# Kernel tuning notes

Measured on AMD Instinct MI355X. Metric: run time of the kernel, lower is better.

## Reference

```python
import jax, jax.numpy as jnp
import numpy as np

D_MODEL = 2048
N_HEAD = 16
HEAD_DIM = D_MODEL // N_HEAD
D_FF = 8192
SEQ = 2048
PAST = 2048
BATCH = 2
LN_EPS = 1e-5


def setup_inputs() -> dict:
    key = jax.random.key(0)
    ks = jax.random.split(key, 16)
    s = 0.02  # weight init scale
    return {
        "x": jax.random.normal(ks[0], (SEQ, BATCH, D_MODEL), jnp.float32),
        "k_cache": jax.random.normal(ks[1], (PAST, BATCH, N_HEAD, HEAD_DIM), jnp.float32),
        "v_cache": jax.random.normal(ks[2], (PAST, BATCH, N_HEAD, HEAD_DIM), jnp.float32),
        "mask": jnp.zeros((SEQ, PAST + SEQ), jnp.float32),
        "q_w": jax.random.normal(ks[3], (D_MODEL, D_MODEL), jnp.float32) * s,
        "q_b": jnp.zeros((D_MODEL,), jnp.float32),
        "k_w": jax.random.normal(ks[4], (D_MODEL, D_MODEL), jnp.float32) * s,
        "k_b": jnp.zeros((D_MODEL,), jnp.float32),
        "v_w": jax.random.normal(ks[5], (D_MODEL, D_MODEL), jnp.float32) * s,
        "v_b": jnp.zeros((D_MODEL,), jnp.float32),
        "o_w": jax.random.normal(ks[6], (D_MODEL, D_MODEL), jnp.float32) * s,
        "o_b": jnp.zeros((D_MODEL,), jnp.float32),
        "ln1_g": jnp.ones((D_MODEL,), jnp.float32),
        "ln1_b": jnp.zeros((D_MODEL,), jnp.float32),
        "ln2_g": jnp.ones((D_MODEL,), jnp.float32),
        "ln2_b": jnp.zeros((D_MODEL,), jnp.float32),
        "w1": jax.random.normal(ks[7], (D_MODEL, D_FF), jnp.float32) * s,
        "b1": jnp.zeros((D_FF,), jnp.float32),
        "w2": jax.random.normal(ks[8], (D_FF, D_MODEL), jnp.float32) * s,
        "b2": jnp.zeros((D_MODEL,), jnp.float32),
    }


def _layernorm(y, g, b):
    m = jnp.mean(y, axis=-1, keepdims=True)
    v = jnp.var(y, axis=-1, keepdims=True)  # biased var, matches torch LayerNorm
    return (y - m) * jax.lax.rsqrt(v + LN_EPS) * g + b


def reference(x, k_cache, v_cache, mask, q_w, q_b, k_w, k_b, v_w, v_b, o_w, o_b,
              ln1_g, ln1_b, ln2_g, ln2_b, w1, b1, w2, b2):
    S, B, D = x.shape
    H, hd = N_HEAD, HEAD_DIM

    x_norm = _layernorm(x, ln1_g, ln1_b)
    q = (x_norm @ q_w + q_b).reshape(S, B, H, hd)
    k = (x_norm @ k_w + k_b).reshape(S, B, H, hd)
    v = (x_norm @ v_w + v_b).reshape(S, B, H, hd)

    k_full = jnp.concatenate([k_cache, k], axis=0)  # [T,B,H,hd], T = past+S
    v_full = jnp.concatenate([v_cache, v], axis=0)

    # scores: [B,H,S,T]
    scores = jnp.einsum('sbhd,tbhd->bhst', q, k_full) / (hd ** 0.5)
    scores = scores + mask  # mask [S,T] broadcasts over B,H
    attn = jax.nn.softmax(scores, axis=-1)
    out = jnp.einsum('bhst,tbhd->sbhd', attn, v_full).reshape(S, B, D)
    x = x + out @ o_w + o_b

    h = _layernorm(x, ln2_g, ln2_b)
    x = x + jax.nn.gelu(h @ w1 + b1, approximate=False) @ w2 + b2
    return (x, k_full, v_full)
```

## Files before the change

### kernel.cpp

```cpp
#include <hip/hip_runtime.h>
#include <hip/hip_bf16.h>


typedef __bf16 bf16x8 __attribute__((ext_vector_type(8)));
typedef float f32x4 __attribute__((ext_vector_type(4)));
typedef float f32x16 __attribute__((ext_vector_type(16)));
typedef unsigned int u32;

__device__ __forceinline__ unsigned short f2bf(float f) {
  union { float f; unsigned u; } v; v.f = f;
  return (unsigned short)((v.u + 0x7FFFu + ((v.u >> 16) & 1u)) >> 16);
}

__device__ __forceinline__ void gl16(const void* g, void* l) {
  __builtin_amdgcn_global_load_lds((__attribute__((address_space(1))) void*)g,
                                   (__attribute__((address_space(3))) void*)l,
                                   16, 0, 0);
}

__global__ __launch_bounds__(256) void ln_k(const float* __restrict__ X,
                                            const float* __restrict__ G,
                                            const float* __restrict__ Bb,
                                            unsigned short* __restrict__ Y) {
  const int row = blockIdx.x;
  const int tid = threadIdx.x;
  const float4* xr = (const float4*)(X + (size_t)row * 2048);
  const float4 xa = xr[tid], xb = xr[tid + 256];
  float s = xa.x + xa.y + xa.z + xa.w + xb.x + xb.y + xb.z + xb.w;
  float q = xa.x * xa.x + xa.y * xa.y + xa.z * xa.z + xa.w * xa.w +
            xb.x * xb.x + xb.y * xb.y + xb.z * xb.z + xb.w * xb.w;
  for (int off = 32; off; off >>= 1) {
    s += __shfl_xor(s, off);
    q += __shfl_xor(q, off);
  }
  __shared__ float red[8];
  const int wv = tid >> 6, ln = tid & 63;
  if (ln == 0) { red[wv] = s; red[4 + wv] = q; }
  __syncthreads();
  s = red[0] + red[1] + red[2] + red[3];
  q = red[4] + red[5] + red[6] + red[7];
  const float mean = s * (1.f / 2048.f);
  const float rstd = rsqrtf(q * (1.f / 2048.f) - mean * mean + 1e-5f);
  const float4 g0 = ((const float4*)G)[tid], g1 = ((const float4*)G)[tid + 256];
  const float4 b0 = ((const float4*)Bb)[tid], b1 = ((const float4*)Bb)[tid + 256];
  ushort4 o0, o1;
  o0.x = f2bf((xa.x - mean) * rstd * g0.x + b0.x);
  o0.y = f2bf((xa.y - mean) * rstd * g0.y + b0.y);
  o0.z = f2bf((xa.z - mean) * rstd * g0.z + b0.z);
  o0.w = f2bf((xa.w - mean) * rstd * g0.w + b0.w);
  o1.x = f2bf((xb.x - mean) * rstd * g1.x + b1.x);
  o1.y = f2bf((xb.y - mean) * rstd * g1.y + b1.y);
  o1.z = f2bf((xb.z - mean) * rstd * g1.z + b1.z);
  o1.w = f2bf((xb.w - mean) * rstd * g1.w + b1.w);
  ((ushort4*)(Y + (size_t)row * 2048))[tid] = o0;
  ((ushort4*)(Y + (size_t)row * 2048))[tid + 256] = o1;
}

__global__ __launch_bounds__(256) void wconvT(const float* __restrict__ W,
                                              unsigned short* __restrict__ Wt,
                                              int K, int N) {
  __shared__ float tl[32][33];
  const int k0 = blockIdx.x * 32, n0 = blockIdx.y * 32;
  const int x = threadIdx.x & 31, y = threadIdx.x >> 5;
  for (int i = 0; i < 4; ++i)
    tl[y + i * 8][x] = W[(size_t)(k0 + y + i * 8) * N + n0 + x];
  __syncthreads();
  for (int i = 0; i < 4; ++i)
    Wt[(size_t)(n0 + y + i * 8) * K + k0 + x] = f2bf(tl[x][y + i * 8]);
}

__global__ __launch_bounds__(256) void kpack(const float* __restrict__ src,
                                             unsigned short* __restrict__ dstb,
                                             float* __restrict__ dstf) {
  const size_t e = ((size_t)blockIdx.x * 256 + threadIdx.x) * 4;
  const int r = (int)(e >> 11), c = (int)(e & 2047);
  const int t = r >> 1, b = r & 1, h = c >> 7, d = c & 127;
  const float4 v = *(const float4*)(src + e);
  ushort4 o;
  o.x = f2bf(v.x); o.y = f2bf(v.y); o.z = f2bf(v.z); o.w = f2bf(v.w);
  *(ushort4*)(dstb + ((size_t)((b * 16 + h) * 4096 + t)) * 128 + d) = o;
  *(float4*)(dstf + (size_t)r * 2048 + c) = v;
}

__global__ __launch_bounds__(256) void vtrans(const float* __restrict__ src,
                                              unsigned short* __restrict__ dstb,
                                              float* __restrict__ dstf) {
  __shared__ float tl[32][33];
  const int bh = blockIdx.z;
  const int b = bh >> 4, h = bh & 15;
  const int t0 = blockIdx.x * 32, d0 = blockIdx.y * 32;
  const int x = threadIdx.x & 31, y = threadIdx.x >> 5;
  for (int i = 0; i < 4; ++i) {
    const int t = t0 + y + i * 8, d = d0 + x;
    const float v = src[((size_t)(t * 2 + b) * 16 + h) * 128 + d];
    tl[y + i * 8][x] = v;
    dstf[((size_t)(t * 2 + b) * 16 + h) * 128 + d] = v;
  }
  __syncthreads();
  for (int i = 0; i < 4; ++i) {
    const int d = d0 + y + i * 8, t = t0 + x;
    dstb[((size_t)bh * 128 + d) * 4096 + t] = f2bf(tl[x][y + i * 8]);
  }
}

__global__ __launch_bounds__(256) void mask0_k(const float* __restrict__ mask,
                                               u32* __restrict__ flags) {
  const float4* p = (const float4*)mask + (size_t)blockIdx.x * 8192 + threadIdx.x;
  int nz = 0;
#pragma unroll
  for (int i = 0; i < 32; ++i) {
    const float4 v = p[i * 256];
    nz |= (v.x != 0.f) | (v.y != 0.f) | (v.z != 0.f) | (v.w != 0.f);
  }
  const int r = __syncthreads_or(nz);
  if (threadIdx.x == 0) flags[blockIdx.x] = (u32)r;
}

template <int TAG, int EPI>
__global__ __launch_bounds__(256) void gemm_bt(
    const unsigned short* __restrict__ A, const unsigned short* __restrict__ Bt,
    const float* __restrict__ bias, const float* __restrict__ Rsd,
    float* __restrict__ Cf, int N, int K) {
  __shared__ unsigned short sA[128 * 64];
  __shared__ unsigned short sB[128 * 64];
  const int tid = threadIdx.x;
  const int wv = tid >> 6, ln = tid & 63;
  const int nwg = gridDim.x;
  const int bid = blockIdx.x;
  const int wk = (bid & 7) * (nwg >> 3) + (bid >> 3);
  const int m0 = (wk & 31) * 128, n0 = (wk >> 5) * 128;
  const int wm = (wv >> 1) * 64, wn = (wv & 1) * 64;
  f32x4 acc[4][4] = {};
  const int nk = K >> 6;
  for (int kt = 0; kt < nk; ++kt) {
    __syncthreads();
#pragma unroll
    for (int c = 0; c < 4; ++c) {
      const int base = (wv * 4 + c) * 1024;
      const int o = base + ln * 16;
      const int row = o >> 7;
      const int xx = o ^ ((row & 7) << 4);
      gl16((const char*)A + ((size_t)(m0 + row) * K + (size_t)kt * 64) * 2 + (xx & 127),
           (char*)sA + base);
      gl16((const char*)Bt + ((size_t)(n0 + row) * K + (size_t)kt * 64) * 2 + (xx & 127),
           (char*)sB + base);
    }
    __syncthreads();
#pragma unroll
    for (int kk = 0; kk < 2; ++kk) {
      bf16x8 af[4], bf[4];
#pragma unroll
      for (int i = 0; i < 4; ++i) {
        const int ra = wm + i * 16 + (ln & 15);
        int aa = (ra << 7) + ((ln >> 4) << 4) + kk * 64;
        aa ^= (ra & 7) << 4;
        af[i] = *(const bf16x8*)((const char*)sA + aa);
        const int rb = wn + i * 16 + (ln & 15);
        int bb = (rb << 7) + ((ln >> 4) << 4) + kk * 64;
        bb ^= (rb & 7) << 4;
        bf[i] = *(const bf16x8*)((const char*)sB + bb);
      }
#pragma unroll
      for (int i = 0; i < 4; ++i)
#pragma unroll
        for (int j = 0; j < 4; ++j)
          acc[i][j] = __builtin_amdgcn_mfma_f32_16x16x32_bf16(af[i], bf[j],
                                                              acc[i][j], 0, 0, 0);
    }
  }
  const int lr = (ln >> 4) << 2, lc = ln & 15;
#pragma unroll
  for (int i = 0; i < 4; ++i) {
#pragma unroll
    for (int j = 0; j < 4; ++j) {
      const int n = n0 + wn + j * 16 + lc;
      const float bv = bias[n];
#pragma unroll
      for (int r = 0; r < 4; ++r) {
        const int m = m0 + wm + i * 16 + lr + r;
        float v = acc[i][j][r] + bv + Rsd[(size_t)m * N + n];
        Cf[(size_t)m * N + n] = v;
      }
    }
  }
}

template <int TAG, int EPI>
__global__ __launch_bounds__(512) void gemm8p(
    const unsigned short* __restrict__ A, const unsigned short* __restrict__ Bt,
    const float* __restrict__ bias, const float* __restrict__ bias2,
    const float* __restrict__ bias3,
    float* __restrict__ Cf, unsigned short* __restrict__ Cb,
    float* __restrict__ of2, unsigned short* __restrict__ pb2,
    unsigned short* __restrict__ pb3, int N, int K) {
  __shared__ unsigned short sA[2][256 * 64];
  __shared__ unsigned short sB[2][256 * 64];
  const int tid = threadIdx.x;
  const int wv = tid >> 6, ln = tid & 63;
  const int wm = wv >> 2, wn = wv & 3;
  const int nwg = gridDim.x;
  const int bid = blockIdx.x;
  const int wk = (bid & 7) * (nwg >> 3) + (bid >> 3);
  const int m0 = (wk & 15) * 256, n0 = (wk >> 4) * 256;
  const int NT = K >> 6, NI = NT >> 1;

  f32x4 acc[8][4] = {};
  bf16x8 af[4][2], bfr[2][2];

  auto ST = [&](int t, int which, int bb) {
    if (t >= NT) return;
    const unsigned short* G = (which < 2) ? A : Bt;
    const int base0 = ((which < 2) ? m0 : n0) + (which & 1) * 128;
    char* dst = (char*)((which < 2) ? &sA[bb][0] : &sB[bb][0]) + (which & 1) * 16384;
    const size_t kb = (size_t)t * 64;
#pragma unroll
    for (int c = 0; c < 2; ++c) {
      const int o = tid * 16 + c * 8192;
      const int row = o >> 7;
      const int cb = (o & 127) ^ ((row & 7) << 4);
      gl16((const char*)G + ((size_t)(base0 + row) * K + kb) * 2 + cb, dst + o);
    }
  };
  auto LDA = [&](int bb, int mh) {
    const char* base = (const char*)&sA[bb][0];
#pragma unroll
    for (int i = 0; i < 4; ++i) {
      const int r = wm * 128 + mh * 64 + i * 16 + (ln & 15);
#pragma unroll
      for (int kk = 0; kk < 2; ++kk) {
        int aa = (r << 7) + ((ln >> 4) << 4) + kk * 64;
        aa ^= (r & 7) << 4;
        af[i][kk] = *(const bf16x8*)(base + aa);
      }
    }
  };
  auto LDB = [&](int bb, int nh) {
    const char* base = (const char*)&sB[bb][0];
#pragma unroll
    for (int j = 0; j < 2; ++j) {
      const int r = wn * 64 + nh * 32 + j * 16 + (ln & 15);
#pragma unroll
      for (int kk = 0; kk < 2; ++kk) {
        int aa = (r << 7) + ((ln >> 4) << 4) + kk * 64;
        aa ^= (r & 7) << 4;
        bfr[j][kk] = *(const bf16x8*)(base + aa);
      }
    }
  };
  auto MM = [&](int mh, int nh) {
    __builtin_amdgcn_s_setprio(1);
#pragma unroll
    for (int i = 0; i < 4; ++i)
#pragma unroll
      for (int j = 0; j < 2; ++j)
#pragma unroll
        for (int kk = 0; kk < 2; ++kk)
          acc[mh * 4 + i][nh * 2 + j] = __builtin_amdgcn_mfma_f32_16x16x32_bf16(
              af[i][kk], bfr[j][kk], acc[mh * 4 + i][nh * 2 + j], 0, 0, 0);
    __builtin_amdgcn_s_setprio(0);
  };
#define BAR() __builtin_amdgcn_s_barrier()
#define VM2() asm volatile("s_waitcnt vmcnt(2)" ::: "memory")
#define VM0() asm volatile("s_waitcnt vmcnt(0)" ::: "memory")

  ST(0, 0, 0); ST(0, 1, 0); ST(0, 2, 0); ST(0, 3, 0); ST(1, 0, 1);
  VM2();
  BAR();

#pragma unroll 1
  for (int it = 0; it < NI; ++it) {
    const int t1 = 2 * it + 1, t2 = 2 * it + 2, t3 = 2 * it + 3;
    const bool lastit = (it == NI - 1);
    LDA(0, 0); LDB(0, 0); ST(t1, 1, 1); BAR(); MM(0, 0); BAR();
    LDB(0, 1);            ST(t1, 2, 1); BAR(); MM(0, 1); BAR();
    LDA(0, 1);            ST(t1, 3, 1); BAR(); MM(1, 1); BAR();
    LDB(0, 0);            ST(t2, 0, 0); BAR(); MM(1, 0);
    if (lastit) VM0(); else VM2();
    BAR();
    LDA(1, 0); LDB(1, 0); ST(t2, 1, 0); BAR(); MM(0, 0); BAR();
    LDB(1, 1);            ST(t2, 2, 0); BAR(); MM(0, 1); BAR();
    LDA(1, 1);            ST(t2, 3, 0); BAR(); MM(1, 1); BAR();
    LDB(1, 0);            ST(t3, 0, 1); BAR(); MM(1, 0);
    if (!lastit) VM2();
    BAR();
  }
#undef BAR
#undef VM2
#undef VM0

  const int lr = (ln >> 4) << 2, lc = ln & 15;
  if (EPI == 0) {
    const int seg = n0 >> 11;
    const float* bp = seg == 0 ? bias : (seg == 1 ? bias2 : bias3);
#pragma unroll
    for (int f = 0; f < 8; ++f) {
#pragma unroll
      for (int j = 0; j < 4; ++j) {
        const int nn = (n0 & 2047) + wn * 64 + j * 16 + lc;
        const int h = nn >> 7, d = nn & 127;
        const float bv = bp[nn];
#pragma unroll
        for (int r = 0; r < 4; ++r) {
          const int m = m0 + wm * 128 + f * 16 + lr + r;
          const int s = m >> 1, b = m & 1;
          const float v = acc[f][j][r] + bv;
          if (seg == 0) {
            Cb[((size_t)(b * 16 + h) * 2048 + s) * 128 + d] = f2bf(v);
          } else if (seg == 1) {
            pb2[((size_t)(b * 16 + h) * 4096 + 2048 + s) * 128 + d] = f2bf(v);
            Cf[((size_t)((2048 + s) * 2 + b) * 16 + h) * 128 + d] = v;
          } else {
            pb3[((size_t)(b * 16 + h) * 128 + d) * 4096 + 2048 + s] = f2bf(v);
            of2[((size_t)((2048 + s) * 2 + b) * 16 + h) * 128 + d] = v;
          }
        }
      }
    }
  } else {
#pragma unroll
    for (int f = 0; f < 8; ++f) {
#pragma unroll
      for (int j = 0; j < 4; ++j) {
        const int n = n0 + wn * 64 + j * 16 + lc;
        const float bv = bias[n];
#pragma unroll
        for (int r = 0; r < 4; ++r) {
          const int m = m0 + wm * 128 + f * 16 + lr + r;
          float v = acc[f][j][r] + bv;
          v = 0.5f * v * (1.f + erff(v * 0.7071067811865476f));
          Cb[(size_t)m * N + n] = f2bf(v);
        }
      }
    }
  }
}

__global__ __launch_bounds__(256, 2) void attn2(
    const unsigned short* __restrict__ Q,
    const unsigned short* __restrict__ Kf,
    const unsigned short* __restrict__ Vt,
    const float* __restrict__ mask,
    const u32* __restrict__ flags,
    unsigned short* __restrict__ ctx) {
  __shared__ unsigned short sK[2][64 * 128];
  __shared__ unsigned short sV[2][128 * 64];
  const int tid = threadIdx.x;
  const int wv = tid >> 6;
  const int ln = tid & 63;
  const int q = ln & 31;
  const int hi = ln >> 5;
  const int sw = (q & 7) << 4;
  const int bh = blockIdx.y;
  const int s0w = blockIdx.x * 128 + wv * 32;

  const int mnz = __syncthreads_or((int)flags[tid]);

  bf16x8 qreg[8];
  {
    const char* qsrc = (const char*)Q +
        ((size_t)bh * 2048 + s0w + q) * 256 + (hi << 4);
#pragma unroll
    for (int kk = 0; kk < 8; ++kk) qreg[kk] = *(const bf16x8*)(qsrc + kk * 32);
  }

  const char* Kc = (const char*)Kf + (size_t)bh * 4096 * 256;
  const char* Vc = (const char*)Vt + (size_t)bh * 128 * 8192;

  auto STAGE = [&](int t0, int bi) {
#pragma unroll
    for (int is = 0; is < 4; ++is) {
      const int oo = tid * 16 + is * 4096;
      const int kr = oo >> 8, kc = oo & 255;
      gl16(Kc + (size_t)(t0 + kr) * 256 + (kc ^ ((kr & 7) << 4)),
           (char*)sK[bi] + oo);
      const int vr = oo >> 7, vc = oo & 127;
      gl16(Vc + (size_t)vr * 8192 + (size_t)t0 * 2 + (vc ^ ((vr & 7) << 4)),
           (char*)sV[bi] + oo);
    }
  };

  f32x16 acc[4] = {};
  float m = -1e30f, l = 0.f;
  const float KLOG = 0.127517445f;

  STAGE(0, 0);
  for (int it = 0; it < 64; ++it) {
    const int cur = it & 1;
    __syncthreads();
    if (it < 63) STAGE((it + 1) * 64, cur ^ 1);

    const char* kb = (const char*)sK[cur];
    const char* vb = (const char*)sV[cur];

    f32x16 sc[2];
#pragma unroll
    for (int st = 0; st < 2; ++st) {
      f32x16 z = {};
      __builtin_amdgcn_s_setprio(1);
#pragma unroll
      for (int kk = 0; kk < 8; ++kk) {
        const bf16x8 kf8 = *(const bf16x8*)(
            kb + (((st * 32 + q) << 8) + (((kk << 5) + (hi << 4)) ^ sw)));
        z = __builtin_amdgcn_mfma_f32_32x32x16_bf16(kf8, qreg[kk], z, 0, 0, 0);
      }
      __builtin_amdgcn_s_setprio(0);
      sc[st] = z;
    }

    if (mnz) {
      const float rs = 11.313708498984761f;
#pragma unroll
      for (int st = 0; st < 2; ++st)
#pragma unroll
        for (int r = 0; r < 16; ++r) {
          const int t = it * 64 + st * 32 + ((r & 3) + ((r >> 2) << 3) + (hi << 2));
          sc[st][r] = fmaf(mask[(size_t)(s0w + q) * 4096 + t], rs, sc[st][r]);
        }
    }

    float pmax = sc[0][0];
#pragma unroll
    for (int st = 0; st < 2; ++st)
#pragma unroll
      for (int r = 0; r < 16; ++r) pmax = fmaxf(pmax, sc[st][r]);
    pmax = fmaxf(pmax, __shfl_xor(pmax, 32));
    if (__any(pmax > m + 90.5f)) {
      const float mn = fmaxf(m, pmax);
      const float corr = exp2f((m - mn) * KLOG);
      m = mn; l *= corr;
#pragma unroll
      for (int d4 = 0; d4 < 4; ++d4)
#pragma unroll
        for (int e = 0; e < 16; ++e) acc[d4][e] *= corr;
    }
    const float mk = m * KLOG;
    float rsum = 0.f;
#pragma unroll
    for (int st = 0; st < 2; ++st)
#pragma unroll
      for (int r = 0; r < 16; ++r) {
        const float e = exp2f(fmaf(sc[st][r], KLOG, -mk));
        sc[st][r] = e;
        rsum += e;
      }
    rsum += __shfl_xor(rsum, 32);
    l += rsum;

    bf16x8 pw[4];
#pragma unroll
    for (int kk = 0; kk < 4; ++kk) {
      const int st = kk >> 1, rb = (kk & 1) * 8;
      u32 w0, w1, w2, w3;
      asm("v_cvt_pk_bf16_f32 %0, %1, %2" : "=v"(w0) : "v"(sc[st][rb + 0]), "v"(sc[st][rb + 1]));
      asm("v_cvt_pk_bf16_f32 %0, %1, %2" : "=v"(w1) : "v"(sc[st][rb + 2]), "v"(sc[st][rb + 3]));
      asm("v_cvt_pk_bf16_f32 %0, %1, %2" : "=v"(w2) : "v"(sc[st][rb + 4]), "v"(sc[st][rb + 5]));
      asm("v_cvt_pk_bf16_f32 %0, %1, %2" : "=v"(w3) : "v"(sc[st][rb + 6]), "v"(sc[st][rb + 7]));
      asm("v_permlane32_swap_b32 %0, %1" : "+v"(w0), "+v"(w2));
      asm("v_permlane32_swap_b32 %0, %1" : "+v"(w1), "+v"(w3));
      union { u32 u[4]; bf16x8 b; } pk;
      pk.u[0] = w0; pk.u[1] = w1; pk.u[2] = w2; pk.u[3] = w3;
      pw[kk] = pk.b;
    }

#pragma unroll
    for (int d4 = 0; d4 < 4; ++d4) {
      __builtin_amdgcn_s_setprio(1);
#pragma unroll
      for (int kk = 0; kk < 4; ++kk) {
        const bf16x8 vf8 = *(const bf16x8*)(
            vb + (((d4 * 32 + q) << 7) + (((kk << 5) + (hi << 4)) ^ sw)));
        acc[d4] = __builtin_amdgcn_mfma_f32_32x32x16_bf16(vf8, pw[kk], acc[d4], 0, 0, 0);
      }
      __builtin_amdgcn_s_setprio(0);
    }
  }

  const float inv = 1.f / l;
  const int b = bh >> 4, h = bh & 15;
  unsigned short* crow = ctx + ((size_t)(s0w + q) * 2 + b) * 2048 + h * 128;
#pragma unroll
  for (int d4 = 0; d4 < 4; ++d4)
#pragma unroll
    for (int r = 0; r < 16; ++r) {
      const int d = d4 * 32 + (r & 3) + ((r >> 2) << 3) + (hi << 2);
      crow[d] = f2bf(acc[d4][r] * inv);
    }
}

extern "C" void kernel_launch(void* const* d_in, const int* in_sizes, int n_in,
                              void* d_out, int out_size, void* d_ws, size_t ws_size,
                              hipStream_t stream) {
  const float* x    = (const float*)d_in[0];
  const float* kc   = (const float*)d_in[1];
  const float* vc   = (const float*)d_in[2];
  const float* mask = (const float*)d_in[3];
  const float* q_w  = (const float*)d_in[4];
  const float* q_b  = (const float*)d_in[5];
  const float* k_w  = (const float*)d_in[6];
  const float* k_b  = (const float*)d_in[7];
  const float* v_w  = (const float*)d_in[8];
  const float* v_b  = (const float*)d_in[9];
  const float* o_w  = (const float*)d_in[10];
  const float* o_b  = (const float*)d_in[11];
  const float* ln1g = (const float*)d_in[12];
  const float* ln1b = (const float*)d_in[13];
  const float* ln2g = (const float*)d_in[14];
  const float* ln2b = (const float*)d_in[15];
  const float* w1   = (const float*)d_in[16];
  const float* b1   = (const float*)d_in[17];
  const float* w2   = (const float*)d_in[18];
  const float* b2   = (const float*)d_in[19];

  float* out_x = (float*)d_out;
  float* out_k = out_x + (size_t)8388608;
  float* out_v = out_k + (size_t)16777216;

  char* ws = (char*)d_ws;
  unsigned short* kf  = (unsigned short*)(ws);
  unsigned short* vft = (unsigned short*)(ws + 33554432);
  unsigned short* Wt  = (unsigned short*)(ws + 67108864);
  float*          x1  = (float*)(ws + 100663296);
  unsigned short* mid = (unsigned short*)ws;

  unsigned short* xn  = (unsigned short*)d_out;
  unsigned short* ctx = xn;
  unsigned short* qb  = (unsigned short*)((char*)d_out + 16777216);
  unsigned short* hn  = qb;
  u32* mflags = (u32*)((char*)d_out + 25165824);

  const dim3 b256(256);

  ln_k<<<4096, b256, 0, stream>>>(x, ln1g, ln1b, xn);
  kpack<<<8192, b256, 0, stream>>>(kc, kf, out_k);
  vtrans<<<dim3(64, 4, 32), b256, 0, stream>>>(vc, vft, out_v);
  mask0_k<<<256, b256, 0, stream>>>(mask, mflags);

  wconvT<<<dim3(64, 64), b256, 0, stream>>>(q_w, Wt, 2048, 2048);
  wconvT<<<dim3(64, 64), b256, 0, stream>>>(k_w, Wt + (size_t)2048 * 2048, 2048, 2048);
  wconvT<<<dim3(64, 64), b256, 0, stream>>>(v_w, Wt + (size_t)4096 * 2048, 2048, 2048);

  gemm8p<0, 0><<<384, dim3(512), 0, stream>>>(
      xn, Wt, q_b, k_b, v_b, out_k, qb, out_v, kf, vft, 6144, 2048);

  attn2<<<dim3(16, 32), b256, 0, stream>>>(qb, kf, vft, mask, mflags, ctx);

  wconvT<<<dim3(64, 64), b256, 0, stream>>>(o_w, Wt, 2048, 2048);
  gemm_bt<1, 1><<<512, b256, 0, stream>>>(ctx, Wt, o_b, x, x1, 2048, 2048);

  ln_k<<<4096, b256, 0, stream>>>(x1, ln2g, ln2b, hn);

  wconvT<<<dim3(64, 256), b256, 0, stream>>>(w1, Wt, 2048, 8192);
  gemm8p<2, 2><<<512, dim3(512), 0, stream>>>(
      hn, Wt, b1, nullptr, nullptr, nullptr, mid, nullptr, nullptr, nullptr,
      8192, 2048);

  wconvT<<<dim3(256, 64), b256, 0, stream>>>(w2, Wt, 8192, 2048);
  gemm_bt<3, 1><<<512, b256, 0, stream>>>(mid, Wt, b2, x1, out_x, 2048, 8192);
}
```

Measured before the change: 980.7 us.

## Add 128x256 pipelined GEMM for QKV/O/FFN2 and halve attention KV tile

Adds a new 512-thread 128x256-tile GEMM with double-buffered LDS, interleaved MFMA phases and a two-blocks-per-CU launch bound. It replaces the simple 128x128 GEMM for the output projection and FFN2, and the 256x256 GEMM for QKV, so the smaller-N GEMMs get more workgroups and better pipelining. The attention kernel now uses 32-key tiles instead of 64 with less LDS and three blocks per CU to raise occupancy, at the cost of twice as many iterations and barriers. The 256x256 kernel is kept only for FFN1 with its GELU epilogue.

```diff
diff --git a/kernel.cpp b/kernel.cpp
--- a/kernel.cpp
+++ b/kernel.cpp
@@ -117,82 +117,10 @@
 }
 
 template <int TAG, int EPI>
-__global__ __launch_bounds__(256) void gemm_bt(
+__global__ __launch_bounds__(512, 2) void gemm8p(
     const unsigned short* __restrict__ A, const unsigned short* __restrict__ Bt,
-    const float* __restrict__ bias, const float* __restrict__ Rsd,
-    float* __restrict__ Cf, int N, int K) {
-  __shared__ unsigned short sA[128 * 64];
-  __shared__ unsigned short sB[128 * 64];
-  const int tid = threadIdx.x;
-  const int wv = tid >> 6, ln = tid & 63;
-  const int nwg = gridDim.x;
-  const int bid = blockIdx.x;
-  const int wk = (bid & 7) * (nwg >> 3) + (bid >> 3);
-  const int m0 = (wk & 31) * 128, n0 = (wk >> 5) * 128;
-  const int wm = (wv >> 1) * 64, wn = (wv & 1) * 64;
-  f32x4 acc[4][4] = {};
-  const int nk = K >> 6;
-  for (int kt = 0; kt < nk; ++kt) {
-    __syncthreads();
-#pragma unroll
-    for (int c = 0; c < 4; ++c) {
-      const int base = (wv * 4 + c) * 1024;
-      const int o = base + ln * 16;
-      const int row = o >> 7;
-      const int xx = o ^ ((row & 7) << 4);
-      gl16((const char*)A + ((size_t)(m0 + row) * K + (size_t)kt * 64) * 2 + (xx & 127),
-           (char*)sA + base);
-      gl16((const char*)Bt + ((size_t)(n0 + row) * K + (size_t)kt * 64) * 2 + (xx & 127),
-           (char*)sB + base);
-    }
-    __syncthreads();
-#pragma unroll
-    for (int kk = 0; kk < 2; ++kk) {
-      bf16x8 af[4], bf[4];
-#pragma unroll
-      for (int i = 0; i < 4; ++i) {
-        const int ra = wm + i * 16 + (ln & 15);
-        int aa = (ra << 7) + ((ln >> 4) << 4) + kk * 64;
-        aa ^= (ra & 7) << 4;
-        af[i] = *(const bf16x8*)((const char*)sA + aa);
-        const int rb = wn + i * 16 + (ln & 15);
-        int bb = (rb << 7) + ((ln >> 4) << 4) + kk * 64;
-        bb ^= (rb & 7) << 4;
-        bf[i] = *(const bf16x8*)((const char*)sB + bb);
-      }
-#pragma unroll
-      for (int i = 0; i < 4; ++i)
-#pragma unroll
-        for (int j = 0; j < 4; ++j)
-          acc[i][j] = __builtin_amdgcn_mfma_f32_16x16x32_bf16(af[i], bf[j],
-                                                              acc[i][j], 0, 0, 0);
-    }
-  }
-  const int lr = (ln >> 4) << 2, lc = ln & 15;
-#pragma unroll
-  for (int i = 0; i < 4; ++i) {
-#pragma unroll
-    for (int j = 0; j < 4; ++j) {
-      const int n = n0 + wn + j * 16 + lc;
-      const float bv = bias[n];
-#pragma unroll
-      for (int r = 0; r < 4; ++r) {
-        const int m = m0 + wm + i * 16 + lr + r;
-        float v = acc[i][j][r] + bv + Rsd[(size_t)m * N + n];
-        Cf[(size_t)m * N + n] = v;
-      }
-    }
-  }
-}
-
-template <int TAG, int EPI>
-__global__ __launch_bounds__(512) void gemm8p(
-    const unsigned short* __restrict__ A, const unsigned short* __restrict__ Bt,
-    const float* __restrict__ bias, const float* __restrict__ bias2,
-    const float* __restrict__ bias3,
-    float* __restrict__ Cf, unsigned short* __restrict__ Cb,
-    float* __restrict__ of2, unsigned short* __restrict__ pb2,
-    unsigned short* __restrict__ pb3, int N, int K) {
+    const float* __restrict__ bias, unsigned short* __restrict__ Cb,
+    int N, int K) {
   __shared__ unsigned short sA[2][256 * 64];
   __shared__ unsigned short sB[2][256 * 64];
   const int tid = threadIdx.x;
@@ -289,11 +217,126 @@
 #undef VM0
 
   const int lr = (ln >> 4) << 2, lc = ln & 15;
+#pragma unroll
+  for (int f = 0; f < 8; ++f) {
+#pragma unroll
+    for (int j = 0; j < 4; ++j) {
+      const int n = n0 + wn * 64 + j * 16 + lc;
+      const float bv = bias[n];
+#pragma unroll
+      for (int r = 0; r < 4; ++r) {
+        const int m = m0 + wm * 128 + f * 16 + lr + r;
+        float v = acc[f][j][r] + bv;
+        v = 0.5f * v * (1.f + erff(v * 0.7071067811865476f));
+        Cb[(size_t)m * N + n] = f2bf(v);
+      }
+    }
+  }
+}
+
+template <int TAG, int EPI>
+__global__ __launch_bounds__(512, 2) void gemm8n(
+    const unsigned short* __restrict__ A, const unsigned short* __restrict__ Bt,
+    const float* __restrict__ bias, const float* __restrict__ bias2,
+    const float* __restrict__ bias3, const float* __restrict__ Rsd,
+    float* __restrict__ Cf, unsigned short* __restrict__ Cb,
+    float* __restrict__ of2, unsigned short* __restrict__ pb2,
+    unsigned short* __restrict__ pb3, int N, int K) {
+  __shared__ unsigned short sA[2][128 * 64];
+  __shared__ unsigned short sB[2][256 * 64];
+  const int tid = threadIdx.x;
+  const int wv = tid >> 6, ln = tid & 63;
+  const int wm = wv >> 2, wn = wv & 3;
+  const int nwg = gridDim.x;
+  const int bid = blockIdx.x;
+  const int wk = (bid & 7) * (nwg >> 3) + (bid >> 3);
+  const int m0 = (wk & 31) * 128, n0 = (wk >> 5) * 256;
+  const int NT = K >> 6;
+
+  f32x4 acc[4][4] = {};
+  bf16x8 af[2][2], bfr[2][2];
+
+  auto ST = [&](int t, int which, int bb) {
+    if (t >= NT) return;
+    const unsigned short* G = (which == 0) ? A : Bt;
+    const int base0 = (which == 0) ? m0 : (which == 1 ? n0 : n0 + 128);
+    char* dst = (which == 0) ? (char*)&sA[bb][0]
+                             : (char*)&sB[bb][0] + (which - 1) * 16384;
+    const size_t kb = (size_t)t * 64;
+#pragma unroll
+    for (int c = 0; c < 2; ++c) {
+      const int o = tid * 16 + c * 8192;
+      const int row = o >> 7;
+      const int cb = (o & 127) ^ ((row & 7) << 4);
+      gl16((const char*)G + ((size_t)(base0 + row) * K + kb) * 2 + cb, dst + o);
+    }
+  };
+  auto LDA = [&](int bb, int mh) {
+    const char* base = (const char*)&sA[bb][0];
+#pragma unroll
+    for (int i = 0; i < 2; ++i) {
+      const int r = wm * 64 + mh * 32 + i * 16 + (ln & 15);
+#pragma unroll
+      for (int kk = 0; kk < 2; ++kk) {
+        int aa = (r << 7) + ((ln >> 4) << 4) + kk * 64;
+        aa ^= (r & 7) << 4;
+        af[i][kk] = *(const bf16x8*)(base + aa);
+      }
+    }
+  };
+  auto LDB = [&](int bb, int nh) {
+    const char* base = (const char*)&sB[bb][0];
+#pragma unroll
+    for (int j = 0; j < 2; ++j) {
+      const int r = wn * 64 + nh * 32 + j * 16 + (ln & 15);
+#pragma unroll
+      for (int kk = 0; kk < 2; ++kk) {
+        int aa = (r << 7) + ((ln >> 4) << 4) + kk * 64;
+        aa ^= (r & 7) << 4;
+        bfr[j][kk] = *(const bf16x8*)(base + aa);
+      }
+    }
+  };
+  auto MM = [&](int mh, int nh) {
+    __builtin_amdgcn_s_setprio(1);
+#pragma unroll
+    for (int i = 0; i < 2; ++i)
+#pragma unroll
+      for (int j = 0; j < 2; ++j)
+#pragma unroll
+        for (int kk = 0; kk < 2; ++kk)
+          acc[mh * 2 + i][nh * 2 + j] = __builtin_amdgcn_mfma_f32_16x16x32_bf16(
+              af[i][kk], bfr[j][kk], acc[mh * 2 + i][nh * 2 + j], 0, 0, 0);
+    __builtin_amdgcn_s_setprio(0);
+  };
+#define BAR() __builtin_amdgcn_s_barrier()
+#define VM2() asm volatile("s_waitcnt vmcnt(2)" ::: "memory")
+#define VM0() asm volatile("s_waitcnt vmcnt(0)" ::: "memory")
+
+  ST(0, 0, 0); ST(0, 1, 0); ST(0, 2, 0); ST(1, 0, 1);
+  VM2();
+  BAR();
+
+#pragma unroll 1
+  for (int t = 0; t < NT; ++t) {
+    const int cur = t & 1;
+    LDA(cur, 0); LDB(cur, 0); ST(t + 1, 1, cur ^ 1); BAR(); MM(0, 0); BAR();
+    LDB(cur, 1); ST(t + 1, 2, cur ^ 1); BAR(); MM(0, 1); BAR();
+    LDA(cur, 1); BAR(); MM(1, 1); BAR();
+    LDB(cur, 0); ST(t + 2, 0, cur); BAR(); MM(1, 0);
+    if (t >= NT - 2) VM0(); else VM2();
+    BAR();
+  }
+#undef BAR
+#undef VM2
+#undef VM0
+
+  const int lr = (ln >> 4) << 2, lc = ln & 15;
   if (EPI == 0) {
     const int seg = n0 >> 11;
     const float* bp = seg == 0 ? bias : (seg == 1 ? bias2 : bias3);
 #pragma unroll
-    for (int f = 0; f < 8; ++f) {
+    for (int i = 0; i < 4; ++i) {
 #pragma unroll
       for (int j = 0; j < 4; ++j) {
         const int nn = (n0 & 2047) + wn * 64 + j * 16 + lc;
@@ -301,9 +344,9 @@
         const float bv = bp[nn];
 #pragma unroll
         for (int r = 0; r < 4; ++r) {
-          const int m = m0 + wm * 128 + f * 16 + lr + r;
+          const int m = m0 + wm * 64 + i * 16 + lr + r;
           const int s = m >> 1, b = m & 1;
-          const float v = acc[f][j][r] + bv;
+          const float v = acc[i][j][r] + bv;
           if (seg == 0) {
             Cb[((size_t)(b * 16 + h) * 2048 + s) * 128 + d] = f2bf(v);
           } else if (seg == 1) {
@@ -318,32 +361,31 @@
     }
   } else {
 #pragma unroll
-    for (int f = 0; f < 8; ++f) {
+    for (int i = 0; i < 4; ++i) {
 #pragma unroll
       for (int j = 0; j < 4; ++j) {
         const int n = n0 + wn * 64 + j * 16 + lc;
         const float bv = bias[n];
 #pragma unroll
         for (int r = 0; r < 4; ++r) {
-          const int m = m0 + wm * 128 + f * 16 + lr + r;
-          float v = acc[f][j][r] + bv;
-          v = 0.5f * v * (1.f + erff(v * 0.7071067811865476f));
-          Cb[(size_t)m * N + n] = f2bf(v);
+          const int m = m0 + wm * 64 + i * 16 + lr + r;
+          const float v = acc[i][j][r] + bv + Rsd[(size_t)m * N + n];
+          Cf[(size_t)m * N + n] = v;
         }
       }
     }
   }
 }
 
-__global__ __launch_bounds__(256, 2) void attn2(
+__global__ __launch_bounds__(256, 3) void attn3(
     const unsigned short* __restrict__ Q,
     const unsigned short* __restrict__ Kf,
     const unsigned short* __restrict__ Vt,
     const float* __restrict__ mask,
     const u32* __restrict__ flags,
     unsigned short* __restrict__ ctx) {
-  __shared__ unsigned short sK[2][64 * 128];
-  __shared__ unsigned short sV[2][128 * 64];
+  __shared__ unsigned short sK[2][32 * 128];
+  __shared__ unsigned short sV[2][128 * 32];
   const int tid = threadIdx.x;
   const int wv = tid >> 6;
   const int ln = tid & 63;
@@ -368,13 +410,13 @@
 
   auto STAGE = [&](int t0, int bi) {
 #pragma unroll
-    for (int is = 0; is < 4; ++is) {
+    for (int is = 0; is < 2; ++is) {
       const int oo = tid * 16 + is * 4096;
       const int kr = oo >> 8, kc = oo & 255;
       gl16(Kc + (size_t)(t0 + kr) * 256 + (kc ^ ((kr & 7) << 4)),
            (char*)sK[bi] + oo);
-      const int vr = oo >> 7, vc = oo & 127;
-      gl16(Vc + (size_t)vr * 8192 + (size_t)t0 * 2 + (vc ^ ((vr & 7) << 4)),
+      const int vr = oo >> 6, vc = oo & 63;
+      gl16(Vc + (size_t)vr * 8192 + (size_t)t0 * 2 + (vc ^ ((vr & 3) << 4)),
            (char*)sV[bi] + oo);
     }
   };
@@ -384,45 +426,40 @@
   const float KLOG = 0.127517445f;
 
   STAGE(0, 0);
-  for (int it = 0; it < 64; ++it) {
+  for (int it = 0; it < 128; ++it) {
     const int cur = it & 1;
     __syncthreads();
-    if (it < 63) STAGE((it + 1) * 64, cur ^ 1);
+    if (it < 127) STAGE((it + 1) * 32, cur ^ 1);
 
     const char* kb = (const char*)sK[cur];
     const char* vb = (const char*)sV[cur];
 
-    f32x16 sc[2];
-#pragma unroll
-    for (int st = 0; st < 2; ++st) {
+    f32x16 sc;
+    {
       f32x16 z = {};
       __builtin_amdgcn_s_setprio(1);
 #pragma unroll
       for (int kk = 0; kk < 8; ++kk) {
         const bf16x8 kf8 = *(const bf16x8*)(
-            kb + (((st * 32 + q) << 8) + (((kk << 5) + (hi << 4)) ^ sw)));
+            kb + ((q << 8) + (((kk << 5) + (hi << 4)) ^ sw)));
         z = __builtin_amdgcn_mfma_f32_32x32x16_bf16(kf8, qreg[kk], z, 0, 0, 0);
       }
       __builtin_amdgcn_s_setprio(0);
-      sc[st] = z;
+      sc = z;
     }
 
     if (mnz) {
       const float rs = 11.313708498984761f;
 #pragma unroll
-      for (int st = 0; st < 2; ++st)
-#pragma unroll
-        for (int r = 0; r < 16; ++r) {
-          const int t = it * 64 + st * 32 + ((r & 3) + ((r >> 2) << 3) + (hi << 2));
-          sc[st][r] = fmaf(mask[(size_t)(s0w + q) * 4096 + t], rs, sc[st][r]);
-        }
-    }
-
-    float pmax = sc[0][0];
-#pragma unroll
-    for (int st = 0; st < 2; ++st)
-#pragma unroll
-      for (int r = 0; r < 16; ++r) pmax = fmaxf(pmax, sc[st][r]);
+      for (int r = 0; r < 16; ++r) {
+        const int t = it * 32 + ((r & 3) + ((r >> 2) << 3) + (hi << 2));
+        sc[r] = fmaf(mask[(size_t)(s0w + q) * 4096 + t], rs, sc[r]);
+      }
+    }
+
+    float pmax = sc[0];
+#pragma unroll
+    for (int r = 1; r < 16; ++r) pmax = fmaxf(pmax, sc[r]);
     pmax = fmaxf(pmax, __shfl_xor(pmax, 32));
     if (__any(pmax > m + 90.5f)) {
       const float mn = fmaxf(m, pmax);
@@ -436,25 +473,23 @@
     const float mk = m * KLOG;
     float rsum = 0.f;
 #pragma unroll
-    for (int st = 0; st < 2; ++st)
-#pragma unroll
-      for (int r = 0; r < 16; ++r) {
-        const float e = exp2f(fmaf(sc[st][r], KLOG, -mk));
-        sc[st][r] = e;
-        rsum += e;
-      }
+    for (int r = 0; r < 16; ++r) {
+      const float e = exp2f(fmaf(sc[r], KLOG, -mk));
+      sc[r] = e;
+      rsum += e;
+    }
     rsum += __shfl_xor(rsum, 32);
     l += rsum;
 
-    bf16x8 pw[4];
-#pragma unroll
-    for (int kk = 0; kk < 4; ++kk) {
-      const int st = kk >> 1, rb = (kk & 1) * 8;
+    bf16x8 pw[2];
+#pragma unroll
+    for (int kk = 0; kk < 2; ++kk) {
+      const int rb = kk * 8;
       u32 w0, w1, w2, w3;
-      asm("v_cvt_pk_bf16_f32 %0, %1, %2" : "=v"(w0) : "v"(sc[st][rb + 0]), "v"(sc[st][rb + 1]));
-      asm("v_cvt_pk_bf16_f32 %0, %1, %2" : "=v"(w1) : "v"(sc[st][rb + 2]), "v"(sc[st][rb + 3]));
-      asm("v_cvt_pk_bf16_f32 %0, %1, %2" : "=v"(w2) : "v"(sc[st][rb + 4]), "v"(sc[st][rb + 5]));
-      asm("v_cvt_pk_bf16_f32 %0, %1, %2" : "=v"(w3) : "v"(sc[st][rb + 6]), "v"(sc[st][rb + 7]));
+      asm("v_cvt_pk_bf16_f32 %0, %1, %2" : "=v"(w0) : "v"(sc[rb + 0]), "v"(sc[rb + 1]));
+      asm("v_cvt_pk_bf16_f32 %0, %1, %2" : "=v"(w1) : "v"(sc[rb + 2]), "v"(sc[rb + 3]));
+      asm("v_cvt_pk_bf16_f32 %0, %1, %2" : "=v"(w2) : "v"(sc[rb + 4]), "v"(sc[rb + 5]));
+      asm("v_cvt_pk_bf16_f32 %0, %1, %2" : "=v"(w3) : "v"(sc[rb + 6]), "v"(sc[rb + 7]));
       asm("v_permlane32_swap_b32 %0, %1" : "+v"(w0), "+v"(w2));
       asm("v_permlane32_swap_b32 %0, %1" : "+v"(w1), "+v"(w3));
       union { u32 u[4]; bf16x8 b; } pk;
@@ -466,9 +501,10 @@
     for (int d4 = 0; d4 < 4; ++d4) {
       __builtin_amdgcn_s_setprio(1);
 #pragma unroll
-      for (int kk = 0; kk < 4; ++kk) {
+      for (int kk = 0; kk < 2; ++kk) {
+        const int vrow = d4 * 32 + q;
         const bf16x8 vf8 = *(const bf16x8*)(
-            vb + (((d4 * 32 + q) << 7) + (((kk << 5) + (hi << 4)) ^ sw)));
+            vb + ((vrow << 6) + (((kk << 5) + (hi << 4)) ^ ((q & 3) << 4))));
         acc[d4] = __builtin_amdgcn_mfma_f32_32x32x16_bf16(vf8, pw[kk], acc[d4], 0, 0, 0);
       }
       __builtin_amdgcn_s_setprio(0);
@@ -539,21 +575,23 @@
   wconvT<<<dim3(64, 64), b256, 0, stream>>>(k_w, Wt + (size_t)2048 * 2048, 2048, 2048);
   wconvT<<<dim3(64, 64), b256, 0, stream>>>(v_w, Wt + (size_t)4096 * 2048, 2048, 2048);
 
-  gemm8p<0, 0><<<384, dim3(512), 0, stream>>>(
-      xn, Wt, q_b, k_b, v_b, out_k, qb, out_v, kf, vft, 6144, 2048);
-
-  attn2<<<dim3(16, 32), b256, 0, stream>>>(qb, kf, vft, mask, mflags, ctx);
+  gemm8n<0, 0><<<768, dim3(512), 0, stream>>>(
+      xn, Wt, q_b, k_b, v_b, nullptr, out_k, qb, out_v, kf, vft, 6144, 2048);
+
+  attn3<<<dim3(16, 32), b256, 0, stream>>>(qb, kf, vft, mask, mflags, ctx);
 
   wconvT<<<dim3(64, 64), b256, 0, stream>>>(o_w, Wt, 2048, 2048);
-  gemm_bt<1, 1><<<512, b256, 0, stream>>>(ctx, Wt, o_b, x, x1, 2048, 2048);
+  gemm8n<1, 1><<<256, dim3(512), 0, stream>>>(
+      ctx, Wt, o_b, nullptr, nullptr, x, x1, nullptr, nullptr, nullptr, nullptr,
+      2048, 2048);
 
   ln_k<<<4096, b256, 0, stream>>>(x1, ln2g, ln2b, hn);
 
   wconvT<<<dim3(64, 256), b256, 0, stream>>>(w1, Wt, 2048, 8192);
-  gemm8p<2, 2><<<512, dim3(512), 0, stream>>>(
-      hn, Wt, b1, nullptr, nullptr, nullptr, mid, nullptr, nullptr, nullptr,
-      8192, 2048);
+  gemm8p<2, 2><<<512, dim3(512), 0, stream>>>(hn, Wt, b1, mid, 8192, 2048);
 
   wconvT<<<dim3(256, 64), b256, 0, stream>>>(w2, Wt, 8192, 2048);
-  gemm_bt<3, 1><<<512, b256, 0, stream>>>(mid, Wt, b2, x1, out_x, 2048, 8192);
-}
+  gemm8n<3, 1><<<256, dim3(512), 0, stream>>>(
+      mid, Wt, b2, nullptr, nullptr, x1, out_x, nullptr, nullptr, nullptr, nullptr,
+      2048, 8192);
+}
```

Result: slower. 1.028 ms (+4.9%).
